# Kernel tuning notes

Measured on AMD Instinct MI355X. Metric: run time of the kernel, lower is better.

## Reference

```python
import jax, jax.numpy as jnp
import numpy as np

NG, ND = 50000, 20000
EG, ED = 300000, 150000
FG = FD = 256
H = 256
FC = 2048
B = 65536
EPS = 1e-5


def _lrelu(x):
    return jnp.where(x >= 0, x, 0.01 * x)


def _bn(x, g, b):
    # BatchNorm1d in training mode: biased batch stats over the node dim
    m = x.mean(axis=0)
    v = ((x - m) ** 2).mean(axis=0)
    return (x - m) * jax.lax.rsqrt(v + EPS) * g + b


def _gconv(x, edge_index, Wr, br, Ws, n_nodes):
    # PyG GraphConv: out = lin_rel(sum_{j->i} x_j) + lin_root(x_i)
    src, dst = edge_index[0], edge_index[1]
    agg = jax.ops.segment_sum(x[src], dst, num_segments=n_nodes)  # [N, in]
    return agg @ Wr + br + x @ Ws


def setup_inputs() -> dict:
    key = jax.random.key(0)
    ks = iter(jax.random.split(key, 64))
    d = {}
    d["gene_x"] = jax.random.normal(next(ks), (NG, FG), jnp.float32)
    d["disease_x"] = jax.random.normal(next(ks), (ND, FD), jnp.float32)
    d["gene_edge_index"] = jax.random.randint(next(ks), (2, EG), 0, NG, jnp.int32)
    d["disease_edge_index"] = jax.random.randint(next(ks), (2, ED), 0, ND, jnp.int32)
    d["batch_idx"] = jax.random.randint(next(ks), (B, 2), 0, ND, jnp.int32)

    def lin(fin, fout):
        s = 1.0 / np.sqrt(fin)
        W = jax.random.uniform(next(ks), (fin, fout), jnp.float32, -s, s)
        b = jax.random.uniform(next(ks), (fout,), jnp.float32, -s, s)
        return W, b

    for p, fin in (("g", FG), ("d", FD)):
        for i in range(3):
            f = fin if i == 0 else H
            Wr, br = lin(f, H)
            Ws, _ = lin(f, H)
            d[f"{p}{i}_Wr"], d[f"{p}{i}_br"], d[f"{p}{i}_Ws"] = Wr, br, Ws
            d[f"bn{p}{i}_g"] = jnp.ones((H,), jnp.float32)
            d[f"bn{p}{i}_b"] = jnp.zeros((H,), jnp.float32)
    d["lin1_W"], d["lin1_b"] = lin(2 * H, FC)
    d["lin2_W"], d["lin2_b"] = lin(FC, FC // 2)
    d["lin3_W"], d["lin3_b"] = lin(FC // 2, FC // 4)
    d["lin4_W"], d["lin4_b"] = lin(FC // 4, 2)
    return d


def reference(gene_x, disease_x, gene_edge_index, disease_edge_index, batch_idx,
              g0_Wr, g0_br, g0_Ws, g1_Wr, g1_br, g1_Ws, g2_Wr, g2_br, g2_Ws,
              d0_Wr, d0_br, d0_Ws, d1_Wr, d1_br, d1_Ws, d2_Wr, d2_br, d2_Ws,
              bng0_g, bng0_b, bng1_g, bng1_b, bng2_g, bng2_b,
              bnd0_g, bnd0_b, bnd1_g, bnd1_b, bnd2_g, bnd2_b,
              lin1_W, lin1_b, lin2_W, lin2_b, lin3_W, lin3_b, lin4_W, lin4_b):
    # gene tower
    g0 = _bn(_lrelu(_gconv(gene_x, gene_edge_index, g0_Wr, g0_br, g0_Ws, NG)), bng0_g, bng0_b)
    g1 = _bn(_lrelu(_gconv(g0, gene_edge_index, g1_Wr, g1_br, g1_Ws, NG)), bng1_g, bng1_b)
    g2 = _bn(_lrelu(_gconv(g1, gene_edge_index, g2_Wr, g2_br, g2_Ws, NG)), bng2_g, bng2_b)
    gene_out = 0.7 * g0 + 0.2 * g1 + 0.1 * g2
    # disease tower
    h0 = _bn(_lrelu(_gconv(disease_x, disease_edge_index, d0_Wr, d0_br, d0_Ws, ND)), bnd0_g, bnd0_b)
    h1 = _bn(_lrelu(_gconv(h0, disease_edge_index, d1_Wr, d1_br, d1_Ws, ND)), bnd1_g, bnd1_b)
    h2 = _bn(_lrelu(_gconv(h1, disease_edge_index, d2_Wr, d2_br, d2_Ws, ND)), bnd2_g, bnd2_b)
    dis_out = 0.7 * h0 + 0.2 * h1 + 0.1 * h2
    # pair gather + MLP head (dropout is identity in eval)
    x = jnp.concatenate([gene_out[batch_idx[:, 0]], dis_out[batch_idx[:, 1]]], axis=1)
    x = _lrelu(x @ lin1_W + lin1_b)
    x = _lrelu(x @ lin2_W + lin2_b)
    x = _lrelu(x @ lin3_W + lin3_b)
    return x @ lin4_W + lin4_b
```

## Files before the change

kernel.cpp:

```cpp
#include <hip/hip_runtime.h>
#include <hip/hip_bf16.h>
#include <cstdint>
#include <cstddef>

#define N_G 50000
#define N_D 20000
#define E_G 300000
#define E_D 150000
#define BATCH 65536

typedef _Float16 f16;
typedef _Float16 f16x8 __attribute__((ext_vector_type(8)));
typedef _Float16 f16x4 __attribute__((ext_vector_type(4)));
typedef float f32x4 __attribute__((ext_vector_type(4)));

__device__ __forceinline__ float clampf(float v) {
    return fminf(fmaxf(v, -60000.f), 60000.f);
}

__device__ __forceinline__ void gl_lds16(const void* g, void* l) {
    __builtin_amdgcn_global_load_lds(
        (const __attribute__((address_space(1))) unsigned int*)g,
        (__attribute__((address_space(3))) unsigned int*)l, 16, 0, 0);
}

__global__ __launch_bounds__(256) void gemm_f16(
    const f16* __restrict__ A,
    const int* __restrict__ bidx,
    const f16* __restrict__ geneT, const f16* __restrict__ disT, int rowBase,
    const f16* __restrict__ Bt, const float* __restrict__ bias,
    f16* __restrict__ C, int M, int N, int K, int relu, int CB, int RB,
    const float* __restrict__ W4, float* __restrict__ outF)
{
    alignas(16) __shared__ f16 sA[128 * 64];
    alignas(16) __shared__ f16 sB[128 * 64];
    const int t = threadIdx.x;
    const int w = t >> 6, l = t & 63;
    const int wm = w >> 1, wn = w & 1;
    const int q = l >> 4, lr = l & 15;

    int flat = blockIdx.x;
    int cb, rb;
    if ((RB & 7) == 0) {
        int x = flat & 7, idx = flat >> 3;
        int Sx = RB >> 3;
        cb = idx % CB;
        rb = x * Sx + idx / CB;
    } else {
        cb = flat % CB;
        rb = flat / CB;
    }
    const int mBase = rb * 128, nBase = cb * 128;

    const int subrow = l >> 3;
    const int c = l & 7;
    const char* pA[4];
    const char* pD[4];
    const char* pB[4];
    const bool fused = (bidx != nullptr);
    const bool concat = (!fused && disT != nullptr);
    const bool twoSrc = fused || concat;
#pragma unroll
    for (int j = 0; j < 4; j++) {
        int seg = j * 4 + w;
        int lrow = seg * 8 + subrow;
        int coff = ((c ^ (lrow & 7)) << 4);
        if (fused) {
            int rg = rowBase + mBase + lrow;
            int gi = bidx[2 * rg], di = bidx[2 * rg + 1];
            pA[j] = (const char*)geneT + (size_t)gi * 512 + coff;
            pD[j] = (const char*)disT + (size_t)di * 512 + coff;
        } else if (concat) {
            int arow = mBase + lrow; if (arow > M - 1) arow = M - 1;
            pA[j] = (const char*)geneT + (size_t)arow * 512 + coff;
            pD[j] = (const char*)disT + (size_t)arow * 512 + coff;
        } else {
            int arow = mBase + lrow; if (arow > M - 1) arow = M - 1;
            pA[j] = (const char*)A + (size_t)arow * K * 2 + coff;
            pD[j] = nullptr;
        }
        int brow = nBase + lrow; if (brow > N - 1) brow = N - 1;
        pB[j] = (const char*)Bt + (size_t)brow * K * 2 + coff;
    }

    f32x4 acc[4][4] = {};

    for (int k0 = 0; k0 < K; k0 += 64) {
        __syncthreads();
#pragma unroll
        for (int j = 0; j < 4; j++) {
            int seg = j * 4 + w;
            const char* srcA;
            if (twoSrc)
                srcA = (k0 < 256) ? (pA[j] + (size_t)k0 * 2) : (pD[j] + (size_t)(k0 - 256) * 2);
            else
                srcA = pA[j] + (size_t)k0 * 2;
            gl_lds16(srcA, sA + seg * 512);
            gl_lds16(pB[j] + (size_t)k0 * 2, sB + seg * 512);
        }
        __syncthreads();
        f16x8 a0[4], a1[4], b0[4], b1[4];
#pragma unroll
        for (int i = 0; i < 4; i++) {
            int r = wm * 64 + i * 16 + lr;
            int rs = r * 64;
            int x0 = (q ^ (r & 7)) << 3;
            int x1 = ((4 + q) ^ (r & 7)) << 3;
            a0[i] = *(const f16x8*)(sA + rs + x0);
            a1[i] = *(const f16x8*)(sA + rs + x1);
        }
#pragma unroll
        for (int jj = 0; jj < 4; jj++) {
            int r = wn * 64 + jj * 16 + lr;
            int rs = r * 64;
            int x0 = (q ^ (r & 7)) << 3;
            int x1 = ((4 + q) ^ (r & 7)) << 3;
            b0[jj] = *(const f16x8*)(sB + rs + x0);
            b1[jj] = *(const f16x8*)(sB + rs + x1);
        }
#pragma unroll
        for (int i = 0; i < 4; i++)
#pragma unroll
            for (int jj = 0; jj < 4; jj++) {
                acc[i][jj] = __builtin_amdgcn_mfma_f32_16x16x32_f16(a0[i], b0[jj], acc[i][jj], 0, 0, 0);
                acc[i][jj] = __builtin_amdgcn_mfma_f32_16x16x32_f16(a1[i], b1[jj], acc[i][jj], 0, 0, 0);
            }
    }

    if (W4 != nullptr) {
        float w40[4], w41[4];
#pragma unroll
        for (int j = 0; j < 4; j++) {
            int col = nBase + wn * 64 + j * 16 + lr;
            w40[j] = W4[col * 2];
            w41[j] = W4[col * 2 + 1];
        }
#pragma unroll
        for (int i = 0; i < 4; i++) {
#pragma unroll
            for (int r = 0; r < 4; r++) {
                int row = mBase + wm * 64 + i * 16 + q * 4 + r;
                float s0 = 0.f, s1 = 0.f;
#pragma unroll
                for (int j = 0; j < 4; j++) {
                    int col = nBase + wn * 64 + j * 16 + lr;
                    float v = acc[i][j][r] + bias[col];
                    v = v >= 0.f ? v : 0.01f * v;
                    v = clampf(v);
                    s0 += v * w40[j];
                    s1 += v * w41[j];
                }
#pragma unroll
                for (int off = 1; off < 16; off <<= 1) {
                    s0 += __shfl_xor(s0, off);
                    s1 += __shfl_xor(s1, off);
                }
                if (lr == 0 && row < M) {
                    atomicAdd(&outF[(size_t)(rowBase + row) * 2], s0);
                    atomicAdd(&outF[(size_t)(rowBase + row) * 2 + 1], s1);
                }
            }
        }
        return;
    }

    __syncthreads();
    f16* lt = ((w >> 1) ? sB : sA) + (w & 1) * 4096;

    float bj[4];
#pragma unroll
    for (int j = 0; j < 4; j++)
        bj[j] = bias ? bias[nBase + wn * 64 + j * 16 + lr] : 0.f;

#pragma unroll
    for (int i = 0; i < 4; i++)
#pragma unroll
        for (int j = 0; j < 4; j++) {
            int col = j * 16 + lr;
#pragma unroll
            for (int r = 0; r < 4; r++) {
                int row = i * 16 + q * 4 + r;
                float v = acc[i][j][r] + bj[j];
                if (relu) v = v >= 0.f ? v : 0.01f * v;
                v = clampf(v);
                int cs = col ^ ((((row >> 2) & 3) << 4) ^ ((row & 3) << 3));
                lt[row * 64 + cs] = (f16)v;
            }
        }
    __syncthreads();

    const int rr = l >> 3;
    const int c8 = l & 7;
#pragma unroll
    for (int it = 0; it < 8; it++) {
        int row = it * 8 + rr;
        int cs = (c8 * 8) ^ ((((row >> 2) & 3) << 4) ^ ((row & 3) << 3));
        f16x8 vv = *(const f16x8*)(lt + row * 64 + cs);
        int grow = mBase + wm * 64 + row;
        if (grow < M)
            *(f16x8*)(C + (size_t)grow * N + nBase + wn * 64 + c8 * 8) = vv;
    }
}

__global__ void cvt_f32_f16(const float* __restrict__ in, f16* __restrict__ out, size_t n) {
    size_t i = ((size_t)blockIdx.x * 256 + threadIdx.x) * 8;
    if (i >= n) return;
    f32x4 a = *(const f32x4*)(in + i);
    f32x4 b = *(const f32x4*)(in + i + 4);
    f16x8 o;
    o[0] = (f16)clampf(a.x); o[1] = (f16)clampf(a.y);
    o[2] = (f16)clampf(a.z); o[3] = (f16)clampf(a.w);
    o[4] = (f16)clampf(b.x); o[5] = (f16)clampf(b.y);
    o[6] = (f16)clampf(b.z); o[7] = (f16)clampf(b.w);
    *(f16x8*)(out + i) = o;
}

__global__ void init_out(const float* __restrict__ b4, float* __restrict__ out, int n) {
    int i = blockIdx.x * 256 + threadIdx.x;
    if (i < n) out[i] = b4[i & 1];
}

__global__ void count_deg(const int* __restrict__ ei, int E, int* __restrict__ deg) {
    int e = blockIdx.x * 256 + threadIdx.x;
    if (e < E) atomicAdd(&deg[ei[E + e]], 1);
}

__global__ void scan_deg(const int* __restrict__ deg, int* __restrict__ rowptr, int Nn) {
    __shared__ int part[1024];
    const int t = threadIdx.x;
    const int C = (Nn + 1023) >> 10;
    const int base = t * C;
    int s = 0;
    for (int i = 0; i < C; i++) { int idx = base + i; if (idx < Nn) s += deg[idx]; }
    part[t] = s;
    __syncthreads();
    for (int off = 1; off < 1024; off <<= 1) {
        int v = (t >= off) ? part[t - off] : 0;
        __syncthreads();
        part[t] += v;
        __syncthreads();
    }
    int pre = (t == 0) ? 0 : part[t - 1];
    for (int i = 0; i < C; i++) {
        int idx = base + i;
        if (idx < Nn) { rowptr[idx] = pre; pre += deg[idx]; }
    }
    if (t == 1023) rowptr[Nn] = part[1023];
}

__global__ void fill_csr(const int* __restrict__ ei, int E, const int* __restrict__ rowptr,
                         int* __restrict__ cursor, int* __restrict__ csr) {
    int e = blockIdx.x * 256 + threadIdx.x;
    if (e < E) {
        int d = ei[E + e];
        int p = rowptr[d] + atomicAdd(&cursor[d], 1);
        csr[p] = ei[e];
    }
}

__global__ void agg_x(const int* __restrict__ rowptr, const int* __restrict__ csr,
                      const f16* __restrict__ X, f16* __restrict__ XA, int Nn) {
    int gid = blockIdx.x * 256 + threadIdx.x;
    int node = gid >> 6, l = gid & 63;
    if (node >= Nn) return;
    int beg = rowptr[node], end = rowptr[node + 1];
    float s0 = 0.f, s1 = 0.f, s2 = 0.f, s3 = 0.f;
    for (int e = beg; e < end; e++) {
        int src = csr[e];
        f16x4 xv = *(const f16x4*)(X + (size_t)src * 256 + l * 4);
        s0 += (float)xv.x; s1 += (float)xv.y; s2 += (float)xv.z; s3 += (float)xv.w;
    }
    f16x4 o;
    o.x = (f16)clampf(s0); o.y = (f16)clampf(s1);
    o.z = (f16)clampf(s2); o.w = (f16)clampf(s3);
    *(f16x4*)(XA + (size_t)node * 256 + l * 4) = o;
}

__global__ void transpose_tile(const float* __restrict__ W, f16* __restrict__ WT,
                               int K, int N, int dstRowOff, int dstColOff, int LK) {
    __shared__ float tile[32][33];
    int n0 = blockIdx.x * 32, k0 = blockIdx.y * 32;
    int tx = threadIdx.x, ty = threadIdx.y;
    for (int yy = ty; yy < 32; yy += 8) {
        int k = k0 + yy, n = n0 + tx;
        tile[yy][tx] = (k < K && n < N) ? W[(size_t)k * N + n] : 0.f;
    }
    __syncthreads();
    for (int yy = ty; yy < 32; yy += 8) {
        int n = n0 + yy, k = k0 + tx;
        if (n < N && k < K)
            WT[(size_t)(dstRowOff + n) * LK + dstColOff + k] = (f16)clampf(tile[tx][yy]);
    }
}

__global__ void colstats(const f16* __restrict__ y, int Nrows, float* __restrict__ stats) {
    int col = threadIdx.x;
    float s = 0, s2 = 0;
    for (int r = blockIdx.x; r < Nrows; r += gridDim.x) {
        float v = (float)y[(size_t)r * 256 + col];
        s += v; s2 += v * v;
    }
    atomicAdd(&stats[col], s);
    atomicAdd(&stats[256 + col], s2);
}

__global__ void bn_apply(f16* __restrict__ y, const float* __restrict__ stats,
                         const float* __restrict__ g, const float* __restrict__ b,
                         float invN, float w, f16* __restrict__ acc, size_t total,
                         int initAcc) {
    size_t i = ((size_t)blockIdx.x * 256 + threadIdx.x) * 8;
    if (i >= total) return;
    int colb = (int)(i & 255);
    f16x8 yv = *(const f16x8*)(y + i);
    f16x8 av = {};
    if (!initAcc) av = *(const f16x8*)(acc + i);
    f16x8 yo, ao;
#pragma unroll
    for (int j = 0; j < 8; j++) {
        int col = colb + j;
        float m = stats[col] * invN;
        float var = stats[256 + col] * invN - m * m;
        if (var < 0.f) var = 0.f;
        float rs = 1.0f / sqrtf(var + 1e-5f);
        float v = ((float)yv[j] - m) * rs * g[col] + b[col];
        v = clampf(v);
        yo[j] = (f16)v;
        float p = initAcc ? 0.f : (float)av[j];
        ao[j] = (f16)clampf(p + w * v);
    }
    *(f16x8*)(y + i) = yo;
    *(f16x8*)(acc + i) = ao;
}

extern "C" void kernel_launch(void* const* d_in, const int* in_sizes, int n_in,
                              void* d_out, int out_size, void* d_ws, size_t ws_size,
                              hipStream_t stream) {
    char* ws = (char*)d_ws;
    size_t off = 0;
    auto alloc = [&](size_t bytes) -> void* {
        void* p = ws + off;
        off += (bytes + 255) & ~(size_t)255;
        return p;
    };

    f16* gene_out = (f16*)alloc((size_t)N_G * 256 * 2);
    f16* dis_out  = (f16*)alloc((size_t)N_D * 256 * 2);
    f16* W1T = (f16*)alloc((size_t)2048 * 512 * 2);
    f16* W2T = (f16*)alloc((size_t)1024 * 2048 * 2);
    f16* W3T = (f16*)alloc((size_t)512 * 1024 * 2);
    f16* WcatT = (f16*)alloc((size_t)256 * 512 * 2);
    int* csr = (int*)alloc((size_t)E_G * 4);
    int* rowptr = (int*)alloc((size_t)(N_G + 1) * 4);
    int* cnt = (int*)alloc((size_t)N_G * 4);
    float* stats = (float*)alloc(512 * 4);

    char* scratch = ws + off;
    size_t avail = (ws_size > off) ? (ws_size - off) : 0;

    f16* ybA = (f16*)scratch;
    f16* ybB = ybA + (size_t)N_G * 256;
    f16* XAbuf = ybB + (size_t)N_G * 256;

    int R = 32768;
    while ((size_t)R * 6144 > avail && R > 256) R >>= 1;
    int chunks = BATCH / R;
    f16* h1 = (f16*)scratch;
    f16* h2 = h1 + (size_t)R * 2048;

    const float* gene_x = (const float*)d_in[0];
    const float* disease_x = (const float*)d_in[1];
    const int* g_ei = (const int*)d_in[2];
    const int* d_ei = (const int*)d_in[3];
    const int* bidx = (const int*)d_in[4];
    float* out = (float*)d_out;

    const float wl[3] = {0.7f, 0.2f, 0.1f};

    auto run_tower = [&](const float* xin, const int* ei, int Nn, int E, int pbase, f16* tout) {
        size_t nelem = (size_t)Nn * 256;
        cvt_f32_f16<<<(int)((nelem / 8 + 255) / 256), 256, 0, stream>>>(xin, ybA, nelem);
        hipMemsetAsync(cnt, 0, (size_t)Nn * 4, stream);
        count_deg<<<(E + 255) / 256, 256, 0, stream>>>(ei, E, cnt);
        scan_deg<<<1, 1024, 0, stream>>>(cnt, rowptr, Nn);
        hipMemsetAsync(cnt, 0, (size_t)Nn * 4, stream);
        fill_csr<<<(E + 255) / 256, 256, 0, stream>>>(ei, E, rowptr, cnt, csr);
        f16* yin = ybA;
        f16* yout = ybB;
        int RB = (Nn + 127) / 128;
        int RBp = (RB + 7) & ~7;
        for (int l = 0; l < 3; l++) {
            const float* Wr = (const float*)d_in[pbase + l * 5 + 0];
            const float* br = (const float*)d_in[pbase + l * 5 + 1];
            const float* Wss = (const float*)d_in[pbase + l * 5 + 2];
            const float* bg = (const float*)d_in[pbase + l * 5 + 3];
            const float* bb = (const float*)d_in[pbase + l * 5 + 4];
            transpose_tile<<<dim3(8, 8), dim3(32, 8), 0, stream>>>(Wss, WcatT, 256, 256, 0, 0, 512);
            transpose_tile<<<dim3(8, 8), dim3(32, 8), 0, stream>>>(Wr, WcatT, 256, 256, 0, 256, 512);
            agg_x<<<(Nn * 64 + 255) / 256, 256, 0, stream>>>(rowptr, csr, yin, XAbuf, Nn);
            gemm_f16<<<2 * RBp, 256, 0, stream>>>(nullptr, nullptr, yin, XAbuf, 0,
                                                  WcatT, br, yout, Nn, 256, 512, 1, 2, RBp,
                                                  nullptr, nullptr);
            hipMemsetAsync(stats, 0, 512 * 4, stream);
            colstats<<<1024, 256, 0, stream>>>(yout, Nn, stats);
            bn_apply<<<(int)((nelem / 8 + 255) / 256), 256, 0, stream>>>(
                yout, stats, bg, bb, 1.0f / Nn, wl[l], tout, nelem, l == 0);
            f16* tmp = yin; yin = yout; yout = tmp;
        }
    };

    run_tower(gene_x, g_ei, N_G, E_G, 5, gene_out);
    run_tower(disease_x, d_ei, N_D, E_D, 20, dis_out);

    const float* lin1_W = (const float*)d_in[35];
    const float* lin1_b = (const float*)d_in[36];
    const float* lin2_W = (const float*)d_in[37];
    const float* lin2_b = (const float*)d_in[38];
    const float* lin3_W = (const float*)d_in[39];
    const float* lin3_b = (const float*)d_in[40];
    const float* lin4_W = (const float*)d_in[41];
    const float* lin4_b = (const float*)d_in[42];

    transpose_tile<<<dim3(64, 16), dim3(32, 8), 0, stream>>>(lin1_W, W1T, 512, 2048, 0, 0, 512);
    transpose_tile<<<dim3(32, 64), dim3(32, 8), 0, stream>>>(lin2_W, W2T, 2048, 1024, 0, 0, 2048);
    transpose_tile<<<dim3(16, 32), dim3(32, 8), 0, stream>>>(lin3_W, W3T, 1024, 512, 0, 0, 1024);
    init_out<<<(BATCH * 2 + 255) / 256, 256, 0, stream>>>(lin4_b, out, BATCH * 2);

    for (int c = 0; c < chunks; c++) {
        int rb = c * R;
        int RB = R / 128;
        gemm_f16<<<16 * RB, 256, 0, stream>>>(nullptr, bidx, gene_out, dis_out, rb,
                                              W1T, lin1_b, h1, R, 2048, 512, 1, 16, RB,
                                              nullptr, nullptr);
        gemm_f16<<<8 * RB, 256, 0, stream>>>(h1, nullptr, nullptr, nullptr, 0,
                                             W2T, lin2_b, h2, R, 1024, 2048, 1, 8, RB,
                                             nullptr, nullptr);
        gemm_f16<<<4 * RB, 256, 0, stream>>>(h2, nullptr, nullptr, nullptr, rb,
                                             W3T, lin3_b, nullptr, R, 512, 1024, 1, 4, RB,
                                             lin4_W, out);
    }
}
```

Baseline: 1.642 ms.

## Add 256x256-tile GEMM for MLP layers and fuse BN column stats into GEMM epilogue

Adds a new 512-thread GEMM kernel with 256x256 output tiles and a double-buffered LDS pipeline. It is used for the first two MLP layers when the chunk size is a multiple of 256, to raise operand reuse per loaded byte. It also fuses the BatchNorm column sum and sum-of-squares into the GNN GEMM epilogue using wave shuffles and atomics, which removes the separate colstats pass over the output. The larger tile uses 128KB of LDS and more accumulator registers, which lowers occupancy. The stats come from fp32 values before f16 rounding, so they differ slightly from the old pass.

```diff
diff --git a/kernel.cpp b/kernel.cpp
--- a/kernel.cpp
+++ b/kernel.cpp
@@ -30,7 +30,8 @@
     const f16* __restrict__ geneT, const f16* __restrict__ disT, int rowBase,
     const f16* __restrict__ Bt, const float* __restrict__ bias,
     f16* __restrict__ C, int M, int N, int K, int relu, int CB, int RB,
-    const float* __restrict__ W4, float* __restrict__ outF)
+    const float* __restrict__ W4, float* __restrict__ outF,
+    float* __restrict__ stats)
 {
     alignas(16) __shared__ f16 sA[128 * 64];
     alignas(16) __shared__ f16 sB[128 * 64];
@@ -172,6 +173,7 @@
     for (int j = 0; j < 4; j++)
         bj[j] = bias ? bias[nBase + wn * 64 + j * 16 + lr] : 0.f;
 
+    float sj[4] = {0.f, 0.f, 0.f, 0.f}, s2j[4] = {0.f, 0.f, 0.f, 0.f};
 #pragma unroll
     for (int i = 0; i < 4; i++)
 #pragma unroll
@@ -183,10 +185,27 @@
                 float v = acc[i][j][r] + bj[j];
                 if (relu) v = v >= 0.f ? v : 0.01f * v;
                 v = clampf(v);
+                if (stats && (mBase + wm * 64 + row) < M) { sj[j] += v; s2j[j] += v * v; }
                 int cs = col ^ ((((row >> 2) & 3) << 4) ^ ((row & 3) << 3));
                 lt[row * 64 + cs] = (f16)v;
             }
         }
+
+    if (stats) {
+#pragma unroll
+        for (int j = 0; j < 4; j++) {
+            float s = sj[j], s2 = s2j[j];
+            s += __shfl_xor(s, 16); s2 += __shfl_xor(s2, 16);
+            s += __shfl_xor(s, 32); s2 += __shfl_xor(s2, 32);
+            if (q == 0) {
+                int col = nBase + wn * 64 + j * 16 + lr;
+                if (col < 256 && col < N) {
+                    atomicAdd(&stats[col], s);
+                    atomicAdd(&stats[256 + col], s2);
+                }
+            }
+        }
+    }
     __syncthreads();
 
     const int rr = l >> 3;
@@ -197,6 +216,146 @@
         int cs = (c8 * 8) ^ ((((row >> 2) & 3) << 4) ^ ((row & 3) << 3));
         f16x8 vv = *(const f16x8*)(lt + row * 64 + cs);
         int grow = mBase + wm * 64 + row;
+        if (grow < M)
+            *(f16x8*)(C + (size_t)grow * N + nBase + wn * 64 + c8 * 8) = vv;
+    }
+}
+
+__global__ __launch_bounds__(512) void gemm256(
+    const f16* __restrict__ A,
+    const int* __restrict__ bidx,
+    const f16* __restrict__ geneT, const f16* __restrict__ disT, int rowBase,
+    const f16* __restrict__ Bt, const float* __restrict__ bias,
+    f16* __restrict__ C, int M, int N, int K, int relu, int CB, int RB)
+{
+    alignas(16) __shared__ f16 sm[65536];
+    const int t = threadIdx.x;
+    const int w = t >> 6, l = t & 63;
+    const int wm = w >> 2, wn = w & 3;
+    const int q = l >> 4, lr = l & 15;
+
+    int flat = blockIdx.x;
+    int cb, rb;
+    if ((RB & 7) == 0) {
+        int x = flat & 7, idx = flat >> 3;
+        int Sx = RB >> 3;
+        cb = idx % CB;
+        rb = x * Sx + idx / CB;
+    } else {
+        cb = flat % CB;
+        rb = flat / CB;
+    }
+    const int mBase = rb * 256, nBase = cb * 256;
+
+    const int subrow = l >> 3;
+    const int c = l & 7;
+    const bool gat = (bidx != nullptr);
+    const char* pA[4];
+    const char* pD[4];
+    const char* pB[4];
+#pragma unroll
+    for (int jj = 0; jj < 4; jj++) {
+        int arow = jj * 64 + w * 8 + subrow;
+        int coff = ((c ^ (arow & 7)) << 4);
+        if (gat) {
+            int rg = rowBase + mBase + arow;
+            int gi = bidx[2 * rg], di = bidx[2 * rg + 1];
+            pA[jj] = (const char*)geneT + (size_t)gi * 512 + coff;
+            pD[jj] = (const char*)disT + (size_t)di * 512 + coff;
+        } else {
+            int ga = mBase + arow; if (ga > M - 1) ga = M - 1;
+            pA[jj] = (const char*)A + (size_t)ga * K * 2 + coff;
+            pD[jj] = nullptr;
+        }
+        int gb = nBase + arow; if (gb > N - 1) gb = N - 1;
+        pB[jj] = (const char*)Bt + (size_t)gb * K * 2 + coff;
+    }
+
+    auto stage = [&](int cbuf, int k0) {
+        f16* bA = sm + cbuf * 32768;
+        f16* bB = bA + 16384;
+#pragma unroll
+        for (int jj = 0; jj < 4; jj++) {
+            int R0 = jj * 64 + w * 8;
+            const char* srcA;
+            if (gat)
+                srcA = (k0 < 256) ? (pA[jj] + (size_t)k0 * 2) : (pD[jj] + (size_t)(k0 - 256) * 2);
+            else
+                srcA = pA[jj] + (size_t)k0 * 2;
+            gl_lds16(srcA, bA + R0 * 64);
+            gl_lds16(pB[jj] + (size_t)k0 * 2, bB + R0 * 64);
+        }
+    };
+
+    f32x4 acc[8][4] = {};
+    const int nkt = K >> 6;
+
+    stage(0, 0);
+    int cur = 0;
+    for (int kt = 0; kt < nkt; kt++) {
+        if (kt + 1 < nkt) {
+            stage(cur ^ 1, (kt + 1) << 6);
+            asm volatile("s_waitcnt vmcnt(8)" ::: "memory");
+        } else {
+            asm volatile("s_waitcnt vmcnt(0)" ::: "memory");
+        }
+        __builtin_amdgcn_s_barrier();
+        __builtin_amdgcn_sched_barrier(0);
+        const f16* bA = sm + cur * 32768;
+        const f16* bB = bA + 16384;
+#pragma unroll
+        for (int ks = 0; ks < 2; ks++) {
+            f16x8 bf[4];
+#pragma unroll
+            for (int nf = 0; nf < 4; nf++) {
+                int rB = wn * 64 + nf * 16 + lr;
+                bf[nf] = *(const f16x8*)(bB + rB * 64 + ((((ks << 2) + q) ^ (rB & 7)) << 3));
+            }
+#pragma unroll
+            for (int mf = 0; mf < 8; mf++) {
+                int rA = wm * 128 + mf * 16 + lr;
+                f16x8 af = *(const f16x8*)(bA + rA * 64 + ((((ks << 2) + q) ^ (rA & 7)) << 3));
+#pragma unroll
+                for (int nf = 0; nf < 4; nf++)
+                    acc[mf][nf] = __builtin_amdgcn_mfma_f32_16x16x32_f16(af, bf[nf], acc[mf][nf], 0, 0, 0);
+            }
+        }
+        __builtin_amdgcn_sched_barrier(0);
+        __builtin_amdgcn_s_barrier();
+        cur ^= 1;
+    }
+    __builtin_amdgcn_sched_barrier(0);
+
+    f16* lt = sm + w * 8192;
+    float bj[4];
+#pragma unroll
+    for (int nf = 0; nf < 4; nf++)
+        bj[nf] = bias ? bias[nBase + wn * 64 + nf * 16 + lr] : 0.f;
+
+#pragma unroll
+    for (int mf = 0; mf < 8; mf++)
+#pragma unroll
+        for (int nf = 0; nf < 4; nf++) {
+            int col = nf * 16 + lr;
+#pragma unroll
+            for (int r = 0; r < 4; r++) {
+                int row = mf * 16 + q * 4 + r;
+                float v = acc[mf][nf][r] + bj[nf];
+                if (relu) v = v >= 0.f ? v : 0.01f * v;
+                v = clampf(v);
+                int cs = col ^ ((((row >> 2) & 3) << 4) ^ ((row & 3) << 3));
+                lt[row * 64 + cs] = (f16)v;
+            }
+        }
+
+    const int rr = l >> 3;
+    const int c8 = l & 7;
+#pragma unroll
+    for (int it = 0; it < 16; it++) {
+        int row = it * 8 + rr;
+        int cs = (c8 * 8) ^ ((((row >> 2) & 3) << 4) ^ ((row & 3) << 3));
+        f16x8 vv = *(const f16x8*)(lt + row * 64 + cs);
+        int grow = mBase + wm * 128 + row;
         if (grow < M)
             *(f16x8*)(C + (size_t)grow * N + nBase + wn * 64 + c8 * 8) = vv;
     }
@@ -291,17 +450,6 @@
         if (n < N && k < K)
             WT[(size_t)(dstRowOff + n) * LK + dstColOff + k] = (f16)clampf(tile[tx][yy]);
     }
-}
-
-__global__ void colstats(const f16* __restrict__ y, int Nrows, float* __restrict__ stats) {
-    int col = threadIdx.x;
-    float s = 0, s2 = 0;
-    for (int r = blockIdx.x; r < Nrows; r += gridDim.x) {
-        float v = (float)y[(size_t)r * 256 + col];
-        s += v; s2 += v * v;
-    }
-    atomicAdd(&stats[col], s);
-    atomicAdd(&stats[256 + col], s2);
 }
 
 __global__ void bn_apply(f16* __restrict__ y, const float* __restrict__ stats,
@@ -397,11 +545,10 @@
             transpose_tile<<<dim3(8, 8), dim3(32, 8), 0, stream>>>(Wss, WcatT, 256, 256, 0, 0, 512);
             transpose_tile<<<dim3(8, 8), dim3(32, 8), 0, stream>>>(Wr, WcatT, 256, 256, 0, 256, 512);
             agg_x<<<(Nn * 64 + 255) / 256, 256, 0, stream>>>(rowptr, csr, yin, XAbuf, Nn);
+            hipMemsetAsync(stats, 0, 512 * 4, stream);
             gemm_f16<<<2 * RBp, 256, 0, stream>>>(nullptr, nullptr, yin, XAbuf, 0,
                                                   WcatT, br, yout, Nn, 256, 512, 1, 2, RBp,
-                                                  nullptr, nullptr);
-            hipMemsetAsync(stats, 0, 512 * 4, stream);
-            colstats<<<1024, 256, 0, stream>>>(yout, Nn, stats);
+                                                  nullptr, nullptr, stats);
             bn_apply<<<(int)((nelem / 8 + 255) / 256), 256, 0, stream>>>(
                 yout, stats, bg, bb, 1.0f / Nn, wl[l], tout, nelem, l == 0);
             f16* tmp = yin; yin = yout; yout = tmp;
@@ -427,15 +574,24 @@
 
     for (int c = 0; c < chunks; c++) {
         int rb = c * R;
+        if ((R & 255) == 0) {
+            int RB2 = R / 256;
+            gemm256<<<8 * RB2, 512, 0, stream>>>(nullptr, bidx, gene_out, dis_out, rb,
+                                                 W1T, lin1_b, h1, R, 2048, 512, 1, 8, RB2);
+            gemm256<<<4 * RB2, 512, 0, stream>>>(h1, nullptr, nullptr, nullptr, 0,
+                                                 W2T, lin2_b, h2, R, 1024, 2048, 1, 4, RB2);
+        } else {
+            int RB = R / 128;
+            gemm_f16<<<16 * RB, 256, 0, stream>>>(nullptr, bidx, gene_out, dis_out, rb,
+                                                  W1T, lin1_b, h1, R, 2048, 512, 1, 16, RB,
+                                                  nullptr, nullptr, nullptr);
+            gemm_f16<<<8 * RB, 256, 0, stream>>>(h1, nullptr, nullptr, nullptr, 0,
+                                                 W2T, lin2_b, h2, R, 1024, 2048, 1, 8, RB,
+                                                 nullptr, nullptr, nullptr);
+        }
         int RB = R / 128;
-        gemm_f16<<<16 * RB, 256, 0, stream>>>(nullptr, bidx, gene_out, dis_out, rb,
-                                              W1T, lin1_b, h1, R, 2048, 512, 1, 16, RB,
-                                              nullptr, nullptr);
-        gemm_f16<<<8 * RB, 256, 0, stream>>>(h1, nullptr, nullptr, nullptr, 0,
-                                             W2T, lin2_b, h2, R, 1024, 2048, 1, 8, RB,
-                                             nullptr, nullptr);
         gemm_f16<<<4 * RB, 256, 0, stream>>>(h2, nullptr, nullptr, nullptr, rb,
                                              W3T, lin3_b, nullptr, R, 512, 1024, 1, 4, RB,
-                                             lin4_W, out);
-    }
-}
+                                             lin4_W, out, nullptr);
+    }
+}
```

Measured after the change: 1.484 ms. -9.6%, faster.

## Fold BatchNorm into next layer weights and fuse column stats into GEMM epilogue

Applied to the files above, without the earlier changes.

Column sum and sum-of-squares for BatchNorm are now accumulated in the GEMM epilogue with shuffles and atomics, which removes the separate colstats pass. The BN affine transform is no longer applied to activations. Its scale is folded into the next layer's transposed weights, and its shift becomes a corrected bias plus a degree-weighted term for the aggregated branch. A final combine3 kernel applies all three BN transforms and the weighted sum in one pass, so the per-layer bn_apply read-modify-write goes away. In exchange it keeps three unnormalized fp16 layer outputs in memory, adds small serial kernels, and stores un-normalized values in fp16, which risks precision loss.

```diff
diff --git a/kernel.cpp b/kernel.cpp
--- a/kernel.cpp
+++ b/kernel.cpp
@@ -30,7 +30,9 @@
     const f16* __restrict__ geneT, const f16* __restrict__ disT, int rowBase,
     const f16* __restrict__ Bt, const float* __restrict__ bias,
     f16* __restrict__ C, int M, int N, int K, int relu, int CB, int RB,
-    const float* __restrict__ W4, float* __restrict__ outF)
+    const float* __restrict__ W4, float* __restrict__ outF,
+    float* __restrict__ stats, const float* __restrict__ c2,
+    const int* __restrict__ deg)
 {
     alignas(16) __shared__ f16 sA[128 * 64];
     alignas(16) __shared__ f16 sB[128 * 64];
@@ -167,26 +169,57 @@
     __syncthreads();
     f16* lt = ((w >> 1) ? sB : sA) + (w & 1) * 4096;
 
-    float bj[4];
-#pragma unroll
-    for (int j = 0; j < 4; j++)
-        bj[j] = bias ? bias[nBase + wn * 64 + j * 16 + lr] : 0.f;
-
-#pragma unroll
-    for (int i = 0; i < 4; i++)
+    float bj[4], c2j[4] = {0.f, 0.f, 0.f, 0.f};
+#pragma unroll
+    for (int j = 0; j < 4; j++) {
+        int col = nBase + wn * 64 + j * 16 + lr;
+        bj[j] = bias ? bias[col] : 0.f;
+        if (c2) c2j[j] = c2[col];
+    }
+
+    float sj[4] = {0.f, 0.f, 0.f, 0.f}, s2j[4] = {0.f, 0.f, 0.f, 0.f};
+#pragma unroll
+    for (int i = 0; i < 4; i++) {
+        float degf[4] = {0.f, 0.f, 0.f, 0.f};
+        if (deg) {
+            int grow0 = mBase + wm * 64 + i * 16 + q * 4;
+#pragma unroll
+            for (int r = 0; r < 4; r++) {
+                int gr = grow0 + r;
+                degf[r] = (gr < M) ? (float)deg[gr] : 0.f;
+            }
+        }
 #pragma unroll
         for (int j = 0; j < 4; j++) {
             int col = j * 16 + lr;
 #pragma unroll
             for (int r = 0; r < 4; r++) {
                 int row = i * 16 + q * 4 + r;
-                float v = acc[i][j][r] + bj[j];
+                float v = acc[i][j][r] + bj[j] + degf[r] * c2j[j];
                 if (relu) v = v >= 0.f ? v : 0.01f * v;
                 v = clampf(v);
+                if (stats && (mBase + wm * 64 + row) < M) { sj[j] += v; s2j[j] += v * v; }
                 int cs = col ^ ((((row >> 2) & 3) << 4) ^ ((row & 3) << 3));
                 lt[row * 64 + cs] = (f16)v;
             }
         }
+    }
+
+    if (stats) {
+#pragma unroll
+        for (int j = 0; j < 4; j++) {
+            float s = sj[j], s2 = s2j[j];
+            s += __shfl_xor(s, 16); s2 += __shfl_xor(s2, 16);
+            s += __shfl_xor(s, 32); s2 += __shfl_xor(s2, 32);
+            if (q == 0) {
+                int col = nBase + wn * 64 + j * 16 + lr;
+                if (col < 256 && col < N) {
+                    atomicAdd(&stats[col], s);
+                    atomicAdd(&stats[256 + col], s2);
+                }
+            }
+        }
+    }
     __syncthreads();
 
     const int rr = l >> 3;
@@ -277,7 +310,8 @@
 }
 
 __global__ void transpose_tile(const float* __restrict__ W, f16* __restrict__ WT,
-                               int K, int N, int dstRowOff, int dstColOff, int LK) {
+                               int K, int N, int dstRowOff, int dstColOff, int LK,
+                               const float* __restrict__ scale) {
     __shared__ float tile[32][33];
     int n0 = blockIdx.x * 32, k0 = blockIdx.y * 32;
     int tx = threadIdx.x, ty = threadIdx.y;
@@ -286,50 +320,60 @@
         tile[yy][tx] = (k < K && n < N) ? W[(size_t)k * N + n] : 0.f;
     }
     __syncthreads();
+    float sc = 1.f;
+    if (scale) { int k = k0 + tx; if (k < K) sc = scale[k]; }
     for (int yy = ty; yy < 32; yy += 8) {
         int n = n0 + yy, k = k0 + tx;
         if (n < N && k < K)
-            WT[(size_t)(dstRowOff + n) * LK + dstColOff + k] = (f16)clampf(tile[tx][yy]);
-    }
-}
-
-__global__ void colstats(const f16* __restrict__ y, int Nrows, float* __restrict__ stats) {
+            WT[(size_t)(dstRowOff + n) * LK + dstColOff + k] = (f16)clampf(tile[tx][yy] * sc);
+    }
+}
+
+__global__ void compute_st(const float* __restrict__ stats, const float* __restrict__ g,
+                           const float* __restrict__ b, float invN, float* __restrict__ st) {
     int col = threadIdx.x;
-    float s = 0, s2 = 0;
-    for (int r = blockIdx.x; r < Nrows; r += gridDim.x) {
-        float v = (float)y[(size_t)r * 256 + col];
-        s += v; s2 += v * v;
-    }
-    atomicAdd(&stats[col], s);
-    atomicAdd(&stats[256 + col], s2);
-}
-
-__global__ void bn_apply(f16* __restrict__ y, const float* __restrict__ stats,
-                         const float* __restrict__ g, const float* __restrict__ b,
-                         float invN, float w, f16* __restrict__ acc, size_t total,
-                         int initAcc) {
+    float m = stats[col] * invN;
+    float var = stats[256 + col] * invN - m * m;
+    if (var < 0.f) var = 0.f;
+    float rs = 1.0f / sqrtf(var + 1e-5f);
+    float s = g[col] * rs;
+    st[col] = s;
+    st[256 + col] = b[col] - m * s;
+}
+
+__global__ void bias_corr(const float* __restrict__ st, const float* __restrict__ Ws,
+                          const float* __restrict__ Wr, const float* __restrict__ br,
+                          float* __restrict__ cbias, float* __restrict__ c2) {
+    int n = threadIdx.x;
+    float s1 = br[n], s2 = 0.f;
+    for (int k = 0; k < 256; k++) {
+        float tk = st[256 + k];
+        s1 += tk * Ws[k * 256 + n];
+        s2 += tk * Wr[k * 256 + n];
+    }
+    cbias[n] = s1;
+    c2[n] = s2;
+}
+
+__global__ void combine3(const f16* __restrict__ y0, const f16* __restrict__ y1,
+                         const f16* __restrict__ y2, const float* __restrict__ stA,
+                         f16* __restrict__ tout, size_t total) {
     size_t i = ((size_t)blockIdx.x * 256 + threadIdx.x) * 8;
     if (i >= total) return;
     int colb = (int)(i & 255);
-    f16x8 yv = *(const f16x8*)(y + i);
-    f16x8 av = {};
-    if (!initAcc) av = *(const f16x8*)(acc + i);
-    f16x8 yo, ao;
+    f16x8 a = *(const f16x8*)(y0 + i);
+    f16x8 b = *(const f16x8*)(y1 + i);
+    f16x8 c = *(const f16x8*)(y2 + i);
+    f16x8 o;
 #pragma unroll
     for (int j = 0; j < 8; j++) {
         int col = colb + j;
-        float m = stats[col] * invN;
-        float var = stats[256 + col] * invN - m * m;
-        if (var < 0.f) var = 0.f;
-        float rs = 1.0f / sqrtf(var + 1e-5f);
-        float v = ((float)yv[j] - m) * rs * g[col] + b[col];
-        v = clampf(v);
-        yo[j] = (f16)v;
-        float p = initAcc ? 0.f : (float)av[j];
-        ao[j] = (f16)clampf(p + w * v);
-    }
-    *(f16x8*)(y + i) = yo;
-    *(f16x8*)(acc + i) = ao;
+        float v = 0.7f * ((float)a[j] * stA[col]        + stA[256 + col])
+                + 0.2f * ((float)b[j] * stA[512 + col]  + stA[768 + col])
+                + 0.1f * ((float)c[j] * stA[1024 + col] + stA[1280 + col]);
+        o[j] = (f16)clampf(v);
+    }
+    *(f16x8*)(tout + i) = o;
 }
 
 extern "C" void kernel_launch(void* const* d_in, const int* in_sizes, int n_in,
@@ -352,14 +396,21 @@
     int* csr = (int*)alloc((size_t)E_G * 4);
     int* rowptr = (int*)alloc((size_t)(N_G + 1) * 4);
     int* cnt = (int*)alloc((size_t)N_G * 4);
-    float* stats = (float*)alloc(512 * 4);
+    int* deg = (int*)alloc((size_t)N_G * 4);
+    float* statsAll = (float*)alloc(3 * 512 * 4);
+    float* stAll = (float*)alloc(3 * 512 * 4);
+    float* cbias = (float*)alloc(256 * 4);
+    float* c2buf = (float*)alloc(256 * 4);
 
     char* scratch = ws + off;
     size_t avail = (ws_size > off) ? (ws_size - off) : 0;
 
-    f16* ybA = (f16*)scratch;
-    f16* ybB = ybA + (size_t)N_G * 256;
-    f16* XAbuf = ybB + (size_t)N_G * 256;
+    const size_t NS = (size_t)N_G * 256;
+    f16* X0 = (f16*)scratch;
+    f16* y0 = X0 + NS;
+    f16* y1 = y0 + NS;
+    f16* y2 = y1 + NS;
+    f16* XAbuf = y2 + NS;
 
     int R = 32768;
     while ((size_t)R * 6144 > avail && R > 256) R >>= 1;
@@ -374,38 +425,48 @@
     const int* bidx = (const int*)d_in[4];
     float* out = (float*)d_out;
 
-    const float wl[3] = {0.7f, 0.2f, 0.1f};
-
     auto run_tower = [&](const float* xin, const int* ei, int Nn, int E, int pbase, f16* tout) {
         size_t nelem = (size_t)Nn * 256;
-        cvt_f32_f16<<<(int)((nelem / 8 + 255) / 256), 256, 0, stream>>>(xin, ybA, nelem);
-        hipMemsetAsync(cnt, 0, (size_t)Nn * 4, stream);
-        count_deg<<<(E + 255) / 256, 256, 0, stream>>>(ei, E, cnt);
-        scan_deg<<<1, 1024, 0, stream>>>(cnt, rowptr, Nn);
+        int nb8 = (int)((nelem / 8 + 255) / 256);
+        cvt_f32_f16<<<nb8, 256, 0, stream>>>(xin, X0, nelem);
+        hipMemsetAsync(deg, 0, (size_t)Nn * 4, stream);
+        count_deg<<<(E + 255) / 256, 256, 0, stream>>>(ei, E, deg);
+        scan_deg<<<1, 1024, 0, stream>>>(deg, rowptr, Nn);
         hipMemsetAsync(cnt, 0, (size_t)Nn * 4, stream);
         fill_csr<<<(E + 255) / 256, 256, 0, stream>>>(ei, E, rowptr, cnt, csr);
-        f16* yin = ybA;
-        f16* yout = ybB;
+        hipMemsetAsync(statsAll, 0, 3 * 512 * 4, stream);
         int RB = (Nn + 127) / 128;
         int RBp = (RB + 7) & ~7;
+        const f16* yin = X0;
+        f16* youts[3] = {y0, y1, y2};
         for (int l = 0; l < 3; l++) {
             const float* Wr = (const float*)d_in[pbase + l * 5 + 0];
             const float* br = (const float*)d_in[pbase + l * 5 + 1];
             const float* Wss = (const float*)d_in[pbase + l * 5 + 2];
             const float* bg = (const float*)d_in[pbase + l * 5 + 3];
             const float* bb = (const float*)d_in[pbase + l * 5 + 4];
-            transpose_tile<<<dim3(8, 8), dim3(32, 8), 0, stream>>>(Wss, WcatT, 256, 256, 0, 0, 512);
-            transpose_tile<<<dim3(8, 8), dim3(32, 8), 0, stream>>>(Wr, WcatT, 256, 256, 0, 256, 512);
+            const float* biasP;
+            const float* c2P;
+            const int* degP;
+            const float* stPrev = (l > 0) ? (stAll + (l - 1) * 512) : nullptr;
+            if (l == 0) {
+                biasP = br; c2P = nullptr; degP = nullptr;
+                transpose_tile<<<dim3(8, 8), dim3(32, 8), 0, stream>>>(Wss, WcatT, 256, 256, 0, 0, 512, nullptr);
+                transpose_tile<<<dim3(8, 8), dim3(32, 8), 0, stream>>>(Wr, WcatT, 256, 256, 0, 256, 512, nullptr);
+            } else {
+                bias_corr<<<1, 256, 0, stream>>>(stPrev, Wss, Wr, br, cbias, c2buf);
+                transpose_tile<<<dim3(8, 8), dim3(32, 8), 0, stream>>>(Wss, WcatT, 256, 256, 0, 0, 512, stPrev);
+                transpose_tile<<<dim3(8, 8), dim3(32, 8), 0, stream>>>(Wr, WcatT, 256, 256, 0, 256, 512, stPrev);
+                biasP = cbias; c2P = c2buf; degP = deg;
+            }
             agg_x<<<(Nn * 64 + 255) / 256, 256, 0, stream>>>(rowptr, csr, yin, XAbuf, Nn);
             gemm_f16<<<2 * RBp, 256, 0, stream>>>(nullptr, nullptr, yin, XAbuf, 0,
-                                                  WcatT, br, yout, Nn, 256, 512, 1, 2, RBp,
-                                                  nullptr, nullptr);
-            hipMemsetAsync(stats, 0, 512 * 4, stream);
-            colstats<<<1024, 256, 0, stream>>>(yout, Nn, stats);
-            bn_apply<<<(int)((nelem / 8 + 255) / 256), 256, 0, stream>>>(
-                yout, stats, bg, bb, 1.0f / Nn, wl[l], tout, nelem, l == 0);
-            f16* tmp = yin; yin = yout; yout = tmp;
-        }
+                                                  WcatT, biasP, youts[l], Nn, 256, 512, 1, 2, RBp,
+                                                  nullptr, nullptr, statsAll + l * 512, c2P, degP);
+            compute_st<<<1, 256, 0, stream>>>(statsAll + l * 512, bg, bb, 1.0f / Nn, stAll + l * 512);
+            yin = youts[l];
+        }
+        combine3<<<nb8, 256, 0, stream>>>(y0, y1, y2, stAll, tout, nelem);
     };
 
     run_tower(gene_x, g_ei, N_G, E_G, 5, gene_out);
@@ -420,9 +481,9 @@
     const float* lin4_W = (const float*)d_in[41];
     const float* lin4_b = (const float*)d_in[42];
 
-    transpose_tile<<<dim3(64, 16), dim3(32, 8), 0, stream>>>(lin1_W, W1T, 512, 2048, 0, 0, 512);
-    transpose_tile<<<dim3(32, 64), dim3(32, 8), 0, stream>>>(lin2_W, W2T, 2048, 1024, 0, 0, 2048);
-    transpose_tile<<<dim3(16, 32), dim3(32, 8), 0, stream>>>(lin3_W, W3T, 1024, 512, 0, 0, 1024);
+    transpose_tile<<<dim3(64, 16), dim3(32, 8), 0, stream>>>(lin1_W, W1T, 512, 2048, 0, 0, 512, nullptr);
+    transpose_tile<<<dim3(32, 64), dim3(32, 8), 0, stream>>>(lin2_W, W2T, 2048, 1024, 0, 0, 2048, nullptr);
+    transpose_tile<<<dim3(16, 32), dim3(32, 8), 0, stream>>>(lin3_W, W3T, 1024, 512, 0, 0, 1024, nullptr);
     init_out<<<(BATCH * 2 + 255) / 256, 256, 0, stream>>>(lin4_b, out, BATCH * 2);
 
     for (int c = 0; c < chunks; c++) {
@@ -430,12 +491,12 @@
         int RB = R / 128;
         gemm_f16<<<16 * RB, 256, 0, stream>>>(nullptr, bidx, gene_out, dis_out, rb,
                                               W1T, lin1_b, h1, R, 2048, 512, 1, 16, RB,
-                                              nullptr, nullptr);
+                                              nullptr, nullptr, nullptr, nullptr, nullptr);
         gemm_f16<<<8 * RB, 256, 0, stream>>>(h1, nullptr, nullptr, nullptr, 0,
                                              W2T, lin2_b, h2, R, 1024, 2048, 1, 8, RB,
-                                             nullptr, nullptr);
+                                             nullptr, nullptr, nullptr, nullptr, nullptr);
         gemm_f16<<<4 * RB, 256, 0, stream>>>(h2, nullptr, nullptr, nullptr, rb,
                                              W3T, lin3_b, nullptr, R, 512, 1024, 1, 4, RB,
-                                             lin4_W, out);
-    }
-}
+                                             lin4_W, out, nullptr, nullptr, nullptr);
+    }
+}
```

After: 1.606 ms. 1.02x faster.
